# Performance work log

Hardware: AMD Instinct MI355X
Metric: run time of the kernel (lower is better)

## Reference

```python
import jax, jax.numpy as jnp
import numpy as np

T, B, D_IN, D_H = 256, 256, 1024, 1024


def setup_inputs() -> dict:
    key = jax.random.key(0)
    k1, k2 = jax.random.split(key)
    seq = jax.random.normal(k1, (T, B, D_IN), dtype=jnp.float32)
    # Kaiming-ish init so tanh does not saturate
    W = jax.random.normal(k2, (D_H, D_IN + D_H), dtype=jnp.float32) / np.sqrt(D_IN + D_H)
    b = jnp.zeros((D_H,), dtype=jnp.float32)
    return {"seq": seq, "W": W, "b": b}


def reference(seq, W, b):
    # seq: (T, B, d_in); W: (d_h, d_in + d_h); b: (d_h,)
    d_h = W.shape[0]
    h0 = jnp.zeros((seq.shape[1], d_h), dtype=seq.dtype)

    def step(h, x):
        # h_{t+1} = tanh(W [h_t ; x_t] + b)
        h_new = jnp.tanh(jnp.concatenate([h, x], axis=-1) @ W.T + b)
        return h_new, h_new

    _, hs = jax.lax.scan(step, h0, seq)  # hs: (T, B, d_h)
    # Original returns the full hidden-state history including the initial zero state
    return jnp.concatenate([h0[None], hs], axis=0)  # (T+1, B, d_h)
```

## Files before the change

kernel.cpp:

```cpp
#include <hip/hip_runtime.h>

#define T_STEPS 256
#define BATCH   256
#define DIN     1024
#define DH      1024

typedef _Float16 half8_t __attribute__((ext_vector_type(8)));
typedef _Float16 half4_t __attribute__((ext_vector_type(4)));
typedef float    f32x4_t __attribute__((ext_vector_type(4)));

#define LDH  1032
#define REDW 68
#define LGW  72
#define LDS_BYTES 37376

#define CPOL_SYS 17

union H4U { half4_t h; unsigned long long u; };

__device__ __forceinline__ float ftanh(float x) {
    float t = x * 2.885390081777927f;
    float e = exp2f(t);
    float r = __builtin_amdgcn_rcpf(e + 1.0f);
    return 1.0f - 2.0f * r;
}

__global__ __launch_bounds__(256) void cvt_w(const float* __restrict__ W,
                                             _Float16* __restrict__ Wh,
                                             _Float16* __restrict__ Wx) {
    const int part = blockIdx.x >> 9;
    size_t base = ((size_t)(blockIdx.x & 511) * 256 + threadIdx.x) * 8;
    const int n = (int)(base >> 10);
    const int k = (int)(base & 1023);
    const float4* s = reinterpret_cast<const float4*>(W + (size_t)n * 2048 + part * 1024 + k);
    float4 a = s[0], b = s[1];
    half8_t h;
    h[0] = (_Float16)a.x; h[1] = (_Float16)a.y;
    h[2] = (_Float16)a.z; h[3] = (_Float16)a.w;
    h[4] = (_Float16)b.x; h[5] = (_Float16)b.y;
    h[6] = (_Float16)b.z; h[7] = (_Float16)b.w;
    _Float16* dst = part ? Wx : Wh;
    *reinterpret_cast<half8_t*>(dst + base) = h;
}

__global__ __launch_bounds__(256) void zero_h0(float* __restrict__ out,
                                               int* __restrict__ flags,
                                               int* __restrict__ zrdy) {
    size_t i = (size_t)blockIdx.x * 256 + threadIdx.x;
    reinterpret_cast<float4*>(out)[i] = make_float4(0.f, 0.f, 0.f, 0.f);
    if (blockIdx.x == 0) {
#pragma unroll
        for (int j = 0; j < 16; ++j)
            __hip_atomic_store(&flags[(int)threadIdx.x * 16 + j], 0,
                               __ATOMIC_RELAXED, __HIP_MEMORY_SCOPE_SYSTEM);
    } else if (blockIdx.x == 1) {
#pragma unroll
        for (int j = 0; j < 16; ++j)
            __hip_atomic_store(&zrdy[(int)threadIdx.x * 16 + j], 0,
                               __ATOMIC_RELAXED, __HIP_MEMORY_SCOPE_SYSTEM);
    }
}

__global__ __launch_bounds__(256, 1) void fused_pipeline(
        const _Float16* __restrict__ Wh,
        const _Float16* __restrict__ Wx,
        const float* __restrict__ bias,
        const float* __restrict__ seq,
        _Float16* __restrict__ Hh,
        int* __restrict__ flags,
        int* __restrict__ zrdy,
        float* __restrict__ out) {
    __shared__ __align__(16) char ldsraw[LDS_BYTES];
    const int tid = threadIdx.x;
    const int bid = blockIdx.x;

    const int wave = tid >> 6;
    const int lane = tid & 63;
    const int fr   = lane & 15;
    const int quad = lane >> 4;

    if (bid >= 256) {
        _Float16* la = reinterpret_cast<_Float16*>(ldsraw);
        _Float16* lb = la + 128 * LGW;

        const int id   = bid - 256;
        const int nblk = (id >> 3) & 7;
        const int mblk = (id & 7) + 8 * (id >> 6);
        const int m0 = mblk * 128;
        const int n0 = nblk * 128;

        const float* __restrict__ X = seq + (size_t)m0 * 1024;
        float* __restrict__ Z = out + (size_t)BATCH * DH + (size_t)m0 * 1024 + n0;

        const int ar = tid >> 1;
        const int kh = tid & 1;
        const float*    Asrc = X  + (size_t)ar * 1024 + kh * 32;
        const _Float16* Bsrc = Wx + (size_t)(n0 + ar) * 1024 + kh * 32;

        float4 af[8];
        uint4  bq[4];
        auto load_tiles = [&](int kb) {
            const float4* s4 = reinterpret_cast<const float4*>(Asrc + kb);
#pragma unroll
            for (int i = 0; i < 8; ++i) af[i] = s4[i];
            const uint4* sb = reinterpret_cast<const uint4*>(Bsrc + kb);
#pragma unroll
            for (int i = 0; i < 4; ++i) bq[i] = sb[i];
        };
        auto store_tiles = [&]() {
#pragma unroll
            for (int j = 0; j < 4; ++j) {
                half8_t h;
                h[0] = (_Float16)af[2 * j].x;     h[1] = (_Float16)af[2 * j].y;
                h[2] = (_Float16)af[2 * j].z;     h[3] = (_Float16)af[2 * j].w;
                h[4] = (_Float16)af[2 * j + 1].x; h[5] = (_Float16)af[2 * j + 1].y;
                h[6] = (_Float16)af[2 * j + 1].z; h[7] = (_Float16)af[2 * j + 1].w;
                *reinterpret_cast<half8_t*>(&la[ar * LGW + kh * 32 + j * 8]) = h;
            }
#pragma unroll
            for (int i = 0; i < 4; ++i)
                *reinterpret_cast<uint4*>(&lb[ar * LGW + kh * 32 + i * 8]) = bq[i];
        };

        const int wm = (wave >> 1) * 64;
        const int wn = (wave & 1) * 64;

        f32x4_t acc[4][4];
#pragma unroll
        for (int i = 0; i < 4; ++i)
#pragma unroll
            for (int j = 0; j < 4; ++j) acc[i][j] = (f32x4_t){0.f, 0.f, 0.f, 0.f};

        load_tiles(0);
#pragma unroll 1
        for (int it = 0; it < 16; ++it) {
            store_tiles();
            __syncthreads();
            if (it < 15) load_tiles((it + 1) * 64);
#pragma unroll
            for (int kk = 0; kk < 2; ++kk) {
                const int ko = kk * 32 + quad * 8;
                half8_t a[4], b[4];
#pragma unroll
                for (int mi = 0; mi < 4; ++mi)
                    a[mi] = *reinterpret_cast<const half8_t*>(
                        &la[(wm + mi * 16 + fr) * LGW + ko]);
#pragma unroll
                for (int ni = 0; ni < 4; ++ni)
                    b[ni] = *reinterpret_cast<const half8_t*>(
                        &lb[(wn + ni * 16 + fr) * LGW + ko]);
#pragma unroll
                for (int mi = 0; mi < 4; ++mi)
#pragma unroll
                    for (int ni = 0; ni < 4; ++ni)
                        acc[mi][ni] = __builtin_amdgcn_mfma_f32_16x16x32_f16(
                            a[mi], b[ni], acc[mi][ni], 0, 0, 0);
            }
            __syncthreads();
        }

#pragma unroll
        for (int ni = 0; ni < 4; ++ni) {
            const float bv = bias[n0 + wn + ni * 16 + fr];
#pragma unroll
            for (int mi = 0; mi < 4; ++mi) {
                const int mr = wm + mi * 16 + quad * 4;
#pragma unroll
                for (int q = 0; q < 4; ++q)
                    __hip_atomic_store(
                        &Z[(size_t)(mr + q) * 1024 + wn + ni * 16 + fr],
                        acc[mi][ni][q] + bv,
                        __ATOMIC_RELAXED, __HIP_MEMORY_SCOPE_SYSTEM);
            }
        }
        __syncthreads();
        if (tid == 0)
            __hip_atomic_store(&zrdy[mblk * 8 + nblk], 1,
                               __ATOMIC_RELAXED, __HIP_MEMORY_SCOPE_SYSTEM);
        return;
    }

    _Float16* hL   = reinterpret_cast<_Float16*>(ldsraw);
    float*    redL = reinterpret_cast<float*>(ldsraw + 16 * LDH * 2);

    const int m = bid & 15;
    const int n = bid >> 4;

    half8_t bfrag[32];
    {
        const _Float16* wp = Wh + (size_t)(n * 64 + wave * 16 + fr) * DH + quad * 8;
#pragma unroll
        for (int ks = 0; ks < 32; ++ks)
            bfrag[ks] = *reinterpret_cast<const half8_t*>(wp + ks * 32);
    }

    const int r  = tid >> 4;
    const int c4 = (tid & 15) * 4;
    const size_t orowg = (size_t)(m * 16 + r);
    int* myflag = flags + (m * 16 + n) * 16;
    const int zcol = n >> 1;
    const int mhalf = m >> 3;

    {
        if (tid == 0) {
            const int* zf = zrdy + (0 + mhalf) * 8 + zcol;
            int g = 0;
            while (!__hip_atomic_load(zf, __ATOMIC_RELAXED,
                                      __HIP_MEMORY_SCOPE_SYSTEM)) {
                if (++g > (1 << 25)) break;
            }
        }
        __syncthreads();

        float* o1 = out + ((size_t)BATCH + orowg) * DH + n * 64 + c4;
        float zv[4];
#pragma unroll
        for (int j = 0; j < 4; ++j)
            zv[j] = __hip_atomic_load(o1 + j, __ATOMIC_RELAXED,
                                      __HIP_MEMORY_SCOPE_SYSTEM);
        float4 v = make_float4(ftanh(zv[0]), ftanh(zv[1]),
                               ftanh(zv[2]), ftanh(zv[3]));
        *reinterpret_cast<float4*>(o1) = v;
        H4U cv;
        cv.h[0] = (_Float16)v.x; cv.h[1] = (_Float16)v.y;
        cv.h[2] = (_Float16)v.z; cv.h[3] = (_Float16)v.w;
        __hip_atomic_store(
            (unsigned long long*)(Hh + ((size_t)BATCH + orowg) * DH + n * 64 + c4),
            cv.u, __ATOMIC_RELAXED, __HIP_MEMORY_SCOPE_SYSTEM);
        __syncthreads();
        if (tid == 0)
            __hip_atomic_store(myflag, 1, __ATOMIC_RELAXED, __HIP_MEMORY_SCOPE_SYSTEM);
    }

    for (int s = 1; s < T_STEPS; ++s) {
        if (tid < 16) {
            const int* f = flags + (m * 16 + tid) * 16;
            int guard = 0;
            while (__hip_atomic_load(f, __ATOMIC_RELAXED,
                                     __HIP_MEMORY_SCOPE_SYSTEM) < s) {
                if (++guard > (1 << 25)) break;
            }
        } else if (tid == 16) {
            const int* zf = zrdy + (2 * s + mhalf) * 8 + zcol;
            int guard = 0;
            while (!__hip_atomic_load(zf, __ATOMIC_RELAXED,
                                      __HIP_MEMORY_SCOPE_SYSTEM)) {
                if (++guard > (1 << 25)) break;
            }
        }
        __syncthreads();

        const _Float16* hsrc = Hh + ((size_t)(s & 1) * BATCH + (size_t)m * 16) * DH;
#pragma unroll
        for (int i = 0; i < 8; ++i) {
            const int c   = wave * 8 + i;
            const int row = c >> 1;
            const int hf  = c & 1;
            const _Float16* src = hsrc + (size_t)row * DH + hf * 512 + lane * 8;
            __builtin_amdgcn_global_load_lds(
                (const __attribute__((address_space(1))) void*)src,
                (__attribute__((address_space(3))) void*)&hL[row * LDH + hf * 512],
                16, 0, CPOL_SYS);
        }
        float* o = out + ((size_t)(s + 1) * BATCH + orowg) * DH + n * 64 + c4;
        float zv[4];
#pragma unroll
        for (int j = 0; j < 4; ++j)
            zv[j] = __hip_atomic_load(o + j, __ATOMIC_RELAXED,
                                      __HIP_MEMORY_SCOPE_SYSTEM);
        __syncthreads();

        f32x4_t acc0 = {0.f, 0.f, 0.f, 0.f}, acc1 = {0.f, 0.f, 0.f, 0.f};
        const _Float16* pa = &hL[fr * LDH + quad * 8];
#pragma unroll
        for (int ks = 0; ks < 16; ++ks) {
            half8_t ae = *reinterpret_cast<const half8_t*>(pa + (2 * ks) * 32);
            half8_t ao = *reinterpret_cast<const half8_t*>(pa + (2 * ks + 1) * 32);
            acc0 = __builtin_amdgcn_mfma_f32_16x16x32_f16(ae, bfrag[2 * ks],     acc0, 0, 0, 0);
            acc1 = __builtin_amdgcn_mfma_f32_16x16x32_f16(ao, bfrag[2 * ks + 1], acc1, 0, 0, 0);
        }
        f32x4_t sum = acc0 + acc1;

#pragma unroll
        for (int q = 0; q < 4; ++q)
            redL[(quad * 4 + q) * REDW + wave * 16 + fr] = sum[q];
        __syncthreads();

        f32x4_t t4 = *reinterpret_cast<const f32x4_t*>(&redL[r * REDW + c4]);
        float4 v = make_float4(ftanh(t4[0] + zv[0]), ftanh(t4[1] + zv[1]),
                               ftanh(t4[2] + zv[2]), ftanh(t4[3] + zv[3]));
        *reinterpret_cast<float4*>(o) = v;
        H4U cv;
        cv.h[0] = (_Float16)v.x; cv.h[1] = (_Float16)v.y;
        cv.h[2] = (_Float16)v.z; cv.h[3] = (_Float16)v.w;
        __hip_atomic_store(
            (unsigned long long*)(Hh + ((size_t)((s + 1) & 1) * BATCH + orowg) * DH
                                  + n * 64 + c4),
            cv.u, __ATOMIC_RELAXED, __HIP_MEMORY_SCOPE_SYSTEM);

        __syncthreads();
        if (tid == 0)
            __hip_atomic_store(myflag, s + 1, __ATOMIC_RELAXED, __HIP_MEMORY_SCOPE_SYSTEM);
    }
}

extern "C" void kernel_launch(void* const* d_in, const int* in_sizes, int n_in,
                              void* d_out, int out_size, void* d_ws, size_t ws_size,
                              hipStream_t stream) {
    const float* seq  = (const float*)d_in[0];
    const float* W    = (const float*)d_in[1];
    const float* bias = (const float*)d_in[2];
    float* out        = (float*)d_out;
    _Float16* Wh      = (_Float16*)d_ws;
    _Float16* Wx      = (_Float16*)d_ws + 1024 * 1024;
    _Float16* Hh      = (_Float16*)d_ws + 2 * 1024 * 1024;
    int* flags        = (int*)((char*)d_ws + 5 * 1024 * 1024);
    int* zrdy         = (int*)((char*)d_ws + 5 * 1024 * 1024 + 16 * 1024);

    hipLaunchKernelGGL(cvt_w, dim3(1024), dim3(256), 0, stream, W, Wh, Wx);
    hipLaunchKernelGGL(zero_h0, dim3(256), dim3(256), 0, stream, out, flags, zrdy);
    hipLaunchKernelGGL(fused_pipeline, dim3(256 + 4096), dim3(256), 0, stream,
                       Wh, Wx, bias, seq, Hh, flags, zrdy, out);
}
```

Measured before the change: 1.333 ms.

## Pre-convert input sequence to fp16 in a separate pass and raise recurrent block priority

Adds a cvt_seq kernel that converts the full fp32 input sequence to fp16 in workspace before the fused pipeline. The input-projection blocks then load fp16 A tiles directly instead of loading fp32 and converting in registers. The goal is to halve the A-tile bytes read inside the persistent pipeline and move conversion off the recurrence's critical path. The cost is an extra full pass over seq (read 256MB, write 128MB) ahead of the main kernel, and a fallback path when the workspace is too small. The recurrent blocks also set s_setprio(1) so they get scheduling priority over the co-resident GEMM blocks.

```diff
diff --git a/kernel.cpp b/kernel.cpp
--- a/kernel.cpp
+++ b/kernel.cpp
@@ -43,6 +43,19 @@
     *reinterpret_cast<half8_t*>(dst + base) = h;
 }
 
+__global__ __launch_bounds__(256) void cvt_seq(const float* __restrict__ seq,
+                                               _Float16* __restrict__ dst) {
+    size_t base = ((size_t)blockIdx.x * 256 + threadIdx.x) * 8;
+    const float4* s = reinterpret_cast<const float4*>(seq + base);
+    float4 a = s[0], b = s[1];
+    half8_t h;
+    h[0] = (_Float16)a.x; h[1] = (_Float16)a.y;
+    h[2] = (_Float16)a.z; h[3] = (_Float16)a.w;
+    h[4] = (_Float16)b.x; h[5] = (_Float16)b.y;
+    h[6] = (_Float16)b.z; h[7] = (_Float16)b.w;
+    *reinterpret_cast<half8_t*>(dst + base) = h;
+}
+
 __global__ __launch_bounds__(256) void zero_h0(float* __restrict__ out,
                                                int* __restrict__ flags,
                                                int* __restrict__ zrdy) {
@@ -61,11 +74,13 @@
     }
 }
 
+template <int A16>
 __global__ __launch_bounds__(256, 1) void fused_pipeline(
         const _Float16* __restrict__ Wh,
         const _Float16* __restrict__ Wx,
         const float* __restrict__ bias,
         const float* __restrict__ seq,
+        const _Float16* __restrict__ seqh,
         _Float16* __restrict__ Hh,
         int* __restrict__ flags,
         int* __restrict__ zrdy,
@@ -89,33 +104,46 @@
         const int m0 = mblk * 128;
         const int n0 = nblk * 128;
 
-        const float* __restrict__ X = seq + (size_t)m0 * 1024;
         float* __restrict__ Z = out + (size_t)BATCH * DH + (size_t)m0 * 1024 + n0;
 
         const int ar = tid >> 1;
         const int kh = tid & 1;
-        const float*    Asrc = X  + (size_t)ar * 1024 + kh * 32;
-        const _Float16* Bsrc = Wx + (size_t)(n0 + ar) * 1024 + kh * 32;
+        const float*    Asrc  = seq  + (size_t)(m0 + ar) * 1024 + kh * 32;
+        const _Float16* Asrch = seqh + (size_t)(m0 + ar) * 1024 + kh * 32;
+        const _Float16* Bsrc  = Wx   + (size_t)(n0 + ar) * 1024 + kh * 32;
 
         float4 af[8];
+        uint4  aq[4];
         uint4  bq[4];
         auto load_tiles = [&](int kb) {
-            const float4* s4 = reinterpret_cast<const float4*>(Asrc + kb);
-#pragma unroll
-            for (int i = 0; i < 8; ++i) af[i] = s4[i];
+            if (A16) {
+                const uint4* sa = reinterpret_cast<const uint4*>(Asrch + kb);
+#pragma unroll
+                for (int i = 0; i < 4; ++i) aq[i] = sa[i];
+            } else {
+                const float4* s4 = reinterpret_cast<const float4*>(Asrc + kb);
+#pragma unroll
+                for (int i = 0; i < 8; ++i) af[i] = s4[i];
+            }
             const uint4* sb = reinterpret_cast<const uint4*>(Bsrc + kb);
 #pragma unroll
             for (int i = 0; i < 4; ++i) bq[i] = sb[i];
         };
         auto store_tiles = [&]() {
-#pragma unroll
-            for (int j = 0; j < 4; ++j) {
-                half8_t h;
-                h[0] = (_Float16)af[2 * j].x;     h[1] = (_Float16)af[2 * j].y;
-                h[2] = (_Float16)af[2 * j].z;     h[3] = (_Float16)af[2 * j].w;
-                h[4] = (_Float16)af[2 * j + 1].x; h[5] = (_Float16)af[2 * j + 1].y;
-                h[6] = (_Float16)af[2 * j + 1].z; h[7] = (_Float16)af[2 * j + 1].w;
-                *reinterpret_cast<half8_t*>(&la[ar * LGW + kh * 32 + j * 8]) = h;
+            if (A16) {
+#pragma unroll
+                for (int i = 0; i < 4; ++i)
+                    *reinterpret_cast<uint4*>(&la[ar * LGW + kh * 32 + i * 8]) = aq[i];
+            } else {
+#pragma unroll
+                for (int j = 0; j < 4; ++j) {
+                    half8_t h;
+                    h[0] = (_Float16)af[2 * j].x;     h[1] = (_Float16)af[2 * j].y;
+                    h[2] = (_Float16)af[2 * j].z;     h[3] = (_Float16)af[2 * j].w;
+                    h[4] = (_Float16)af[2 * j + 1].x; h[5] = (_Float16)af[2 * j + 1].y;
+                    h[6] = (_Float16)af[2 * j + 1].z; h[7] = (_Float16)af[2 * j + 1].w;
+                    *reinterpret_cast<half8_t*>(&la[ar * LGW + kh * 32 + j * 8]) = h;
+                }
             }
 #pragma unroll
             for (int i = 0; i < 4; ++i)
@@ -179,6 +207,8 @@
                                __ATOMIC_RELAXED, __HIP_MEMORY_SCOPE_SYSTEM);
         return;
     }
+
+    __builtin_amdgcn_s_setprio(1);
 
     _Float16* hL   = reinterpret_cast<_Float16*>(ldsraw);
     float*    redL = reinterpret_cast<float*>(ldsraw + 16 * LDH * 2);
@@ -316,9 +346,19 @@
     _Float16* Hh      = (_Float16*)d_ws + 2 * 1024 * 1024;
     int* flags        = (int*)((char*)d_ws + 5 * 1024 * 1024);
     int* zrdy         = (int*)((char*)d_ws + 5 * 1024 * 1024 + 16 * 1024);
+    _Float16* seqh    = (_Float16*)((char*)d_ws + 6 * 1024 * 1024);
+
+    const size_t need = 6ull * 1024 * 1024
+                      + (size_t)T_STEPS * BATCH * DIN * sizeof(_Float16);
 
     hipLaunchKernelGGL(cvt_w, dim3(1024), dim3(256), 0, stream, W, Wh, Wx);
     hipLaunchKernelGGL(zero_h0, dim3(256), dim3(256), 0, stream, out, flags, zrdy);
-    hipLaunchKernelGGL(fused_pipeline, dim3(256 + 4096), dim3(256), 0, stream,
-                       Wh, Wx, bias, seq, Hh, flags, zrdy, out);
-}
+    if (ws_size >= need) {
+        hipLaunchKernelGGL(cvt_seq, dim3(32768), dim3(256), 0, stream, seq, seqh);
+        hipLaunchKernelGGL(fused_pipeline<1>, dim3(256 + 4096), dim3(256), 0, stream,
+                           Wh, Wx, bias, seq, seqh, Hh, flags, zrdy, out);
+    } else {
+        hipLaunchKernelGGL(fused_pipeline<0>, dim3(256 + 4096), dim3(256), 0, stream,
+                           Wh, Wx, bias, seq, seqh, Hh, flags, zrdy, out);
+    }
+}
```

Measured after the change: 1.444 ms. 1.08x slower.
